# Optimization experiments

Hardware: AMD Instinct MI355X
Metric: run time of the kernel (lower is better)

The kernel has to match this reference:

```python
import jax, jax.numpy as jnp
import numpy as np
from jax import lax

EPS = 1e-05


def rmsnorm_axis1(x, w, eps=EPS):
    # RMS over channel axis (axis=1), scale by per-channel weight
    ms = jnp.mean(x * x, axis=1, keepdims=True)
    return x * lax.rsqrt(ms + eps) * w[None, :, None]


def dwconv1d(x, w, b, dilation):
    # x: [B, C, L]; w: [C, 1, K] depthwise (feature_group_count=C)
    pad = (w.shape[-1] - 1) // 2 * dilation
    y = lax.conv_general_dilated(
        x, w, window_strides=(1,), padding=[(pad, pad)],
        rhs_dilation=(dilation,), dimension_numbers=('NCH', 'OIH', 'NCH'),
        feature_group_count=x.shape[1])
    return y + b[None, :, None]


def setup_inputs() -> dict:
    key = jax.random.key(0)
    ks = jax.random.split(key, 12)
    B, C, L, K = 16, 512, 2048, 3
    s = 1.0 / np.sqrt(C)
    return {
        'number_log': jax.random.normal(ks[0], (B,), jnp.float32),
        'x': jax.random.normal(ks[1], (B, C, L), jnp.float32),
        'pre_w': jnp.ones((C,), jnp.float32),
        'conv_w': jax.random.normal(ks[2], (C, 1, K), jnp.float32) * 0.3,
        'conv_b': jnp.zeros((C,), jnp.float32),
        'conv1_w': jax.random.normal(ks[3], (C, 1, K), jnp.float32) * 0.3,
        'conv1_b': jnp.zeros((C,), jnp.float32),
        'conv2_w': jax.random.normal(ks[4], (C, 1, K), jnp.float32) * 0.3,
        'conv2_b': jnp.zeros((C,), jnp.float32),
        'gate_w': jax.random.normal(ks[5], (C, C), jnp.float32) * s,
        'gate_b': jnp.zeros((C,), jnp.float32),
        'post_w': jnp.ones((C,), jnp.float32),
        'logits_w': jax.random.normal(ks[6], (1, C, 1), jnp.float32) * s,
    }


def reference(number_log, x, pre_w, conv_w, conv_b, conv1_w, conv1_b,
              conv2_w, conv2_b, gate_w, gate_b, post_w, logits_w):
    # pre_norm over channel axis
    x_norm = rmsnorm_axis1(x, pre_w)
    # three dilated depthwise conv branches, summed
    x_d = (dwconv1d(x_norm, conv_w, conv_b, 1)
           + dwconv1d(x_norm, conv1_w, conv1_b, 2)
           + dwconv1d(x_norm, conv2_w, conv2_b, 4))
    # gate: Linear over channel dim of transposed input, SiLU
    gate = jax.nn.silu(jnp.einsum('bcl,dc->bdl', x_norm, gate_w)
                       + gate_b[None, :, None])
    x_d = rmsnorm_axis1(x_d * gate, post_w)
    # logits: 1x1 conv C->1, no bias
    out = jnp.einsum('bcl,oc->bol', x + x_d, logits_w[:, :, 0])
    return out
```

## Files before the change

kernel.cpp:

```cpp
#include <hip/hip_runtime.h>
#include <hip/hip_bf16.h>

#define BB 16
#define CC 512
#define LL 2048

typedef float f32x4 __attribute__((ext_vector_type(4)));
typedef short s16x8 __attribute__((ext_vector_type(8)));

static __device__ __forceinline__ float bf2f(unsigned short u) {
    union { unsigned int i; float f; } v; v.i = ((unsigned int)u) << 16; return v.f;
}
static __device__ __forceinline__ unsigned short f2bf(float f) {
    union { float fv; unsigned int i; } v; v.fv = f;
    unsigned int x = v.i;
    return (unsigned short)((x + 0x7FFFu + ((x >> 16) & 1u)) >> 16);
}

__global__ void k0_cast(const float* __restrict__ gw, unsigned short* __restrict__ gwb) {
    int i = blockIdx.x * 256 + threadIdx.x;
    if (i < CC * CC) gwb[i] = f2bf(gw[i]);
}

#define K1_ST 524
__global__ __launch_bounds__(256) void k1_rms_t(
    const float* __restrict__ x, const float* __restrict__ pre_w,
    unsigned short* __restrict__ xnt, float* __restrict__ invr) {
    __shared__ float tile[32 * K1_ST];
    __shared__ float red[32 * 33];
    __shared__ float pwS[CC];
    __shared__ float ivS[32];
    const int tid = threadIdx.x;
    const int b  = blockIdx.x >> 6;
    const int lt = blockIdx.x & 63;
    const int l0 = lt * 32;
    const float* xb = x + (size_t)(b * CC) * LL + l0;

    for (int i = tid; i < CC; i += 256) pwS[i] = pre_w[i];

    const int lq = tid & 7;
    const int cr = tid >> 3;
    f32x4 ssq = {0.f, 0.f, 0.f, 0.f};
    #pragma unroll
    for (int p = 0; p < 16; ++p) {
        int c = p * 32 + cr;
        f32x4 v = *(const f32x4*)(xb + (size_t)c * LL + lq * 4);
        #pragma unroll
        for (int r = 0; r < 4; ++r) {
            ssq[r] += v[r] * v[r];
            tile[(lq * 4 + r) * K1_ST + c] = v[r];
        }
    }
    #pragma unroll
    for (int r = 0; r < 4; ++r) red[(lq * 4 + r) * 33 + cr] = ssq[r];
    __syncthreads();
    if (tid < 32) {
        float s = 0.f;
        #pragma unroll
        for (int g = 0; g < 32; ++g) s += red[tid * 33 + g];
        float iv = rsqrtf(s * (1.0f / CC) + 1e-5f);
        ivS[tid] = iv;
        invr[b * LL + l0 + tid] = iv;
    }
    __syncthreads();
    unsigned short* xo = xnt + ((size_t)b * LL + l0) * CC;
    #pragma unroll
    for (int p = 0; p < 16; ++p) {
        int q = p * 256 + tid;
        int l = q >> 7, cq = (q & 127) * 4;
        f32x4 t = *(const f32x4*)&tile[l * K1_ST + cq];
        f32x4 w = *(const f32x4*)&pwS[cq];
        float iv = ivS[l];
        ushort4 o;
        o.x = f2bf(t[0] * iv * w[0]);
        o.y = f2bf(t[1] * iv * w[1]);
        o.z = f2bf(t[2] * iv * w[2]);
        o.w = f2bf(t[3] * iv * w[3]);
        *(ushort4*)(xo + (size_t)l * CC + cq) = o;
    }
}

__global__ __launch_bounds__(512) void k2_gemm(
    const unsigned short* __restrict__ gwb,
    const unsigned short* __restrict__ xnt,
    const float* __restrict__ gate_b,
    unsigned short* __restrict__ gate) {
    __shared__ unsigned short As[2][256 * 64];
    __shared__ unsigned short Bs[2][256 * 64];
    const int tid = threadIdx.x;
    const int w = tid >> 6, lane = tid & 63;
    const int lo = lane & 15, hi = lane >> 4;
    const int wm = w >> 2, wn = w & 3;
    const int nt = blockIdx.x, mt = blockIdx.y, b = blockIdx.z;
    const int m0 = mt * 256, n0 = nt * 256;
    const unsigned short* Ab = gwb;
    const unsigned short* Bb = xnt + (size_t)b * LL * CC;

    #define K2_STAGE(buf, kt)                                                        \
        {                                                                            \
            int k0_ = (kt) * 64;                                                     \
            _Pragma("unroll")                                                        \
            for (int s = 0; s < 4; ++s) {                                            \
                int g = tid + s * 512;                                               \
                int row = g >> 3, col8 = (g & 7) * 8;                                \
                __builtin_amdgcn_global_load_lds(                                    \
                    (const __attribute__((address_space(1))) void*)(Ab + (size_t)(m0 + row) * CC + k0_ + col8), \
                    (__attribute__((address_space(3))) void*)(&As[buf][g * 8]),      \
                    16, 0, 0);                                                       \
                __builtin_amdgcn_global_load_lds(                                    \
                    (const __attribute__((address_space(1))) void*)(Bb + (size_t)(n0 + row) * CC + k0_ + col8), \
                    (__attribute__((address_space(3))) void*)(&Bs[buf][g * 8]),      \
                    16, 0, 0);                                                       \
            }                                                                        \
        }

    f32x4 acc[8][4] = {};
    K2_STAGE(0, 0);
    __syncthreads();

    for (int kt = 0; kt < 8; ++kt) {
        const int cur = kt & 1;
        if (kt < 7) K2_STAGE(cur ^ 1, kt + 1);
        #pragma unroll
        for (int kk = 0; kk < 2; ++kk) {
            s16x8 af[8], bf[4];
            #pragma unroll
            for (int mi = 0; mi < 8; ++mi)
                af[mi] = *(const s16x8*)(&As[cur][(wm * 128 + mi * 16 + lo) * 64 + kk * 32 + hi * 8]);
            #pragma unroll
            for (int ni = 0; ni < 4; ++ni)
                bf[ni] = *(const s16x8*)(&Bs[cur][(wn * 64 + ni * 16 + lo) * 64 + kk * 32 + hi * 8]);
            #pragma unroll
            for (int mi = 0; mi < 8; ++mi)
                #pragma unroll
                for (int ni = 0; ni < 4; ++ni)
                    acc[mi][ni] = __builtin_amdgcn_mfma_f32_16x16x32_bf16(
                        af[mi], bf[ni], acc[mi][ni], 0, 0, 0);
        }
        __syncthreads();
    }

    #pragma unroll
    for (int mi = 0; mi < 8; ++mi) {
        #pragma unroll
        for (int ni = 0; ni < 4; ++ni) {
            int n = n0 + wn * 64 + ni * 16 + lo;
            int d0 = m0 + wm * 128 + mi * 16 + hi * 4;
            #pragma unroll
            for (int r = 0; r < 4; ++r) {
                int d = d0 + r;
                float z = acc[mi][ni][r] + gate_b[d];
                float s = z / (1.0f + __expf(-z));
                gate[((size_t)(b * CC + d)) * LL + n] = f2bf(s);
            }
        }
    }
}

__global__ __launch_bounds__(256) void k3a(
    const float* __restrict__ x, const float* __restrict__ invr,
    const unsigned short* __restrict__ gate,
    const float* __restrict__ cw0, const float* __restrict__ cb0,
    const float* __restrict__ cw1, const float* __restrict__ cb1,
    const float* __restrict__ cw2, const float* __restrict__ cb2,
    const float* __restrict__ pre_w, const float* __restrict__ post_w,
    const float* __restrict__ lw, float* __restrict__ part) {
    __shared__ float tapS[64][8];
    __shared__ float biasS[64], preS[64], lwS[64], pwlwS[64];
    __shared__ float ivs[136];
    __shared__ float red[8][128][3];
    const int tid = threadIdx.x;
    const int lt = blockIdx.x;
    const int cc = blockIdx.y;
    const int b  = blockIdx.z;
    const int l0 = lt * 128;
    const int c0 = cc * 64;

    if (tid < 64) {
        int c = c0 + tid;
        float w10 = cw0[c*3], w11 = cw0[c*3+1], w12 = cw0[c*3+2];
        float w20 = cw1[c*3], w21 = cw1[c*3+1], w22 = cw1[c*3+2];
        float w40 = cw2[c*3], w41 = cw2[c*3+1], w42 = cw2[c*3+2];
        tapS[tid][0] = w40; tapS[tid][1] = w20; tapS[tid][2] = w10;
        tapS[tid][3] = w11 + w21 + w41;
        tapS[tid][4] = w12; tapS[tid][5] = w22; tapS[tid][6] = w42;
        biasS[tid] = cb0[c] + cb1[c] + cb2[c];
        preS[tid]  = pre_w[c];
        float lwc = lw[c];
        lwS[tid] = lwc;
        pwlwS[tid] = post_w[c] * lwc;
    }
    if (tid < 136) {
        int lg = l0 - 4 + tid;
        ivs[tid] = (lg >= 0 && lg < LL) ? invr[b * LL + lg] : 0.f;
    }
    __syncthreads();

    const int li = tid & 31, ci = tid >> 5;
    const int lq = l0 + li * 4;
    float iv[12];
    #pragma unroll
    for (int j = 0; j < 12; ++j) iv[j] = ivs[li * 4 + j];

    const int ia = (lq - 4 < 0) ? 0 : lq - 4;
    const int ic = (lq + 4 > LL - 4) ? LL - 4 : lq + 4;

    float ass[4] = {}, adp[4] = {}, adx[4] = {};
    const float* xbase = x + ((size_t)(b * CC + c0)) * LL;
    const unsigned short* gbase = gate + ((size_t)(b * CC + c0)) * LL;

    #pragma unroll
    for (int j = 0; j < 8; ++j) {
        const int cl = ci * 8 + j;
        const float* xr = xbase + (size_t)cl * LL;
        f32x4 xa = *(const f32x4*)(xr + ia);
        f32x4 xm = *(const f32x4*)(xr + lq);
        f32x4 xc = *(const f32x4*)(xr + ic);
        uint2 gu = *(const uint2*)(gbase + (size_t)cl * LL + lq);
        float g[4];
        g[0] = bf2f((unsigned short)(gu.x & 0xffff));
        g[1] = bf2f((unsigned short)(gu.x >> 16));
        g[2] = bf2f((unsigned short)(gu.y & 0xffff));
        g[3] = bf2f((unsigned short)(gu.y >> 16));
        float z[12];
        #pragma unroll
        for (int r = 0; r < 4; ++r) {
            z[r]     = xa[r] * iv[r];
            z[r + 4] = xm[r] * iv[r + 4];
            z[r + 8] = xc[r] * iv[r + 8];
        }
        const float t0 = tapS[cl][0], t1 = tapS[cl][1], t2 = tapS[cl][2],
                    t3 = tapS[cl][3], t4 = tapS[cl][4], t5 = tapS[cl][5],
                    t6 = tapS[cl][6];
        const float pre = preS[cl], bias = biasS[cl], pwlw = pwlwS[cl], lwc = lwS[cl];
        #pragma unroll
        for (int k = 0; k < 4; ++k) {
            float s = t0 * z[k] + t1 * z[k + 2] + t2 * z[k + 3] + t3 * z[k + 4]
                    + t4 * z[k + 5] + t5 * z[k + 6] + t6 * z[k + 8];
            float p = (pre * s + bias) * g[k];
            ass[k] += p * p;
            adp[k] += p * pwlw;
            adx[k] += xm[k] * lwc;
        }
    }
    #pragma unroll
    for (int k = 0; k < 4; ++k) {
        red[ci][li * 4 + k][0] = ass[k];
        red[ci][li * 4 + k][1] = adp[k];
        red[ci][li * 4 + k][2] = adx[k];
    }
    __syncthreads();
    if (tid < 128) {
        float s0 = 0.f, s1 = 0.f, s2 = 0.f;
        #pragma unroll
        for (int g2 = 0; g2 < 8; ++g2) {
            s0 += red[g2][tid][0];
            s1 += red[g2][tid][1];
            s2 += red[g2][tid][2];
        }
        float* pp = part + (((size_t)(b * 8 + cc)) * LL + l0 + tid) * 3;
        pp[0] = s0; pp[1] = s1; pp[2] = s2;
    }
}

__global__ __launch_bounds__(256) void k3b(
    const float* __restrict__ part, float* __restrict__ out) {
    int gl = blockIdx.x * 256 + threadIdx.x;
    int b = gl >> 11, l = gl & 2047;
    float s0 = 0.f, s1 = 0.f, s2 = 0.f;
    #pragma unroll
    for (int cc2 = 0; cc2 < 8; ++cc2) {
        const float* pp = part + (((size_t)(b * 8 + cc2)) * LL + l) * 3;
        s0 += pp[0]; s1 += pp[1]; s2 += pp[2];
    }
    out[gl] = s2 + rsqrtf(s0 * (1.0f / CC) + 1e-5f) * s1;
}

extern "C" void kernel_launch(void* const* d_in, const int* in_sizes, int n_in,
                              void* d_out, int out_size, void* d_ws, size_t ws_size,
                              hipStream_t stream) {
    const float* x      = (const float*)d_in[1];
    const float* pre_w  = (const float*)d_in[2];
    const float* cw0    = (const float*)d_in[3];
    const float* cb0    = (const float*)d_in[4];
    const float* cw1    = (const float*)d_in[5];
    const float* cb1    = (const float*)d_in[6];
    const float* cw2    = (const float*)d_in[7];
    const float* cb2    = (const float*)d_in[8];
    const float* gw     = (const float*)d_in[9];
    const float* gb     = (const float*)d_in[10];
    const float* post_w = (const float*)d_in[11];
    const float* lw     = (const float*)d_in[12];
    float* out = (float*)d_out;

    char* ws = (char*)d_ws;
    unsigned short* gwb  = (unsigned short*)(ws);
    unsigned short* xnt  = (unsigned short*)(ws + 524288);
    float*          invr = (float*)(ws + 524288 + 33554432);
    unsigned short* gate = (unsigned short*)(ws + 524288 + 33554432 + 131072);
    float*          part = (float*)(ws + 524288);

    hipLaunchKernelGGL(k0_cast,  dim3((CC * CC + 255) / 256), dim3(256), 0, stream, gw, gwb);
    hipLaunchKernelGGL(k1_rms_t, dim3(BB * (LL / 32)),        dim3(256), 0, stream, x, pre_w, xnt, invr);
    hipLaunchKernelGGL(k2_gemm,  dim3(LL / 256, CC / 256, BB), dim3(512), 0, stream, gwb, xnt, gb, gate);
    hipLaunchKernelGGL(k3a,      dim3(LL / 128, CC / 64, BB), dim3(256), 0, stream,
                       x, invr, gate, cw0, cb0, cw1, cb1, cw2, cb2, pre_w, post_w, lw, part);
    hipLaunchKernelGGL(k3b,      dim3(BB * LL / 256),         dim3(256), 0, stream, part, out);
}
```

Before: 85.23 us.

## Stage k1 tile in bf16 and software-pipeline the gate GEMM with swizzled LDS

k1 now stores the transposed tile in LDS as bf16 instead of fp32, which halves shared memory and lets the output pass move 8-element vectors. This adds an extra rounding of x before normalisation. The gate GEMM splits each k-step into four phases that interleave LDS fragment reads, async global-to-LDS prefetch of the next tile, and MFMA bursts under raised wave priority, with explicit barriers and waitcnts. It also XOR-swizzles the LDS k offsets to cut bank conflicts and requests 2 blocks per CU in the launch bounds, which may raise register pressure.

```diff
diff --git a/kernel.cpp b/kernel.cpp
--- a/kernel.cpp
+++ b/kernel.cpp
@@ -22,11 +22,11 @@
     if (i < CC * CC) gwb[i] = f2bf(gw[i]);
 }
 
-#define K1_ST 524
+#define K1_ST 520
 __global__ __launch_bounds__(256) void k1_rms_t(
     const float* __restrict__ x, const float* __restrict__ pre_w,
     unsigned short* __restrict__ xnt, float* __restrict__ invr) {
-    __shared__ float tile[32 * K1_ST];
+    __shared__ unsigned short tile[32 * K1_ST];
     __shared__ float red[32 * 33];
     __shared__ float pwS[CC];
     __shared__ float ivS[32];
@@ -48,7 +48,7 @@
         #pragma unroll
         for (int r = 0; r < 4; ++r) {
             ssq[r] += v[r] * v[r];
-            tile[(lq * 4 + r) * K1_ST + c] = v[r];
+            tile[(lq * 4 + r) * K1_ST + c] = f2bf(v[r]);
         }
     }
     #pragma unroll
@@ -65,22 +65,24 @@
     __syncthreads();
     unsigned short* xo = xnt + ((size_t)b * LL + l0) * CC;
     #pragma unroll
-    for (int p = 0; p < 16; ++p) {
-        int q = p * 256 + tid;
-        int l = q >> 7, cq = (q & 127) * 4;
-        f32x4 t = *(const f32x4*)&tile[l * K1_ST + cq];
-        f32x4 w = *(const f32x4*)&pwS[cq];
+    for (int p = 0; p < 8; ++p) {
+        int g = p * 256 + tid;
+        int l = g >> 6, c8 = (g & 63) * 8;
+        s16x8 t = *(const s16x8*)&tile[l * K1_ST + c8];
+        f32x4 w0 = *(const f32x4*)&pwS[c8];
+        f32x4 w1 = *(const f32x4*)&pwS[c8 + 4];
         float iv = ivS[l];
-        ushort4 o;
-        o.x = f2bf(t[0] * iv * w[0]);
-        o.y = f2bf(t[1] * iv * w[1]);
-        o.z = f2bf(t[2] * iv * w[2]);
-        o.w = f2bf(t[3] * iv * w[3]);
-        *(ushort4*)(xo + (size_t)l * CC + cq) = o;
-    }
-}
-
-__global__ __launch_bounds__(512) void k2_gemm(
+        s16x8 o;
+        #pragma unroll
+        for (int r = 0; r < 4; ++r) {
+            o[r]     = (short)f2bf(bf2f((unsigned short)t[r])     * iv * w0[r]);
+            o[r + 4] = (short)f2bf(bf2f((unsigned short)t[r + 4]) * iv * w1[r]);
+        }
+        *(s16x8*)(xo + (size_t)l * CC + c8) = o;
+    }
+}
+
+__global__ __launch_bounds__(512, 2) void k2_gemm(
     const unsigned short* __restrict__ gwb,
     const unsigned short* __restrict__ xnt,
     const float* __restrict__ gate_b,
@@ -96,48 +98,70 @@
     const unsigned short* Ab = gwb;
     const unsigned short* Bb = xnt + (size_t)b * LL * CC;
 
-    #define K2_STAGE(buf, kt)                                                        \
+    #define K2_STG(pp, buf, kt_)                                                     \
         {                                                                            \
-            int k0_ = (kt) * 64;                                                     \
-            _Pragma("unroll")                                                        \
-            for (int s = 0; s < 4; ++s) {                                            \
-                int g = tid + s * 512;                                               \
-                int row = g >> 3, col8 = (g & 7) * 8;                                \
-                __builtin_amdgcn_global_load_lds(                                    \
-                    (const __attribute__((address_space(1))) void*)(Ab + (size_t)(m0 + row) * CC + k0_ + col8), \
-                    (__attribute__((address_space(3))) void*)(&As[buf][g * 8]),      \
-                    16, 0, 0);                                                       \
-                __builtin_amdgcn_global_load_lds(                                    \
-                    (const __attribute__((address_space(1))) void*)(Bb + (size_t)(n0 + row) * CC + k0_ + col8), \
-                    (__attribute__((address_space(3))) void*)(&Bs[buf][g * 8]),      \
-                    16, 0, 0);                                                       \
-            }                                                                        \
+            int g = (pp) * 512 + tid;                                                \
+            int row = g >> 3;                                                        \
+            int ks = ((g & 7) * 8) ^ ((row & 4) ? 16 : 0);                           \
+            __builtin_amdgcn_global_load_lds(                                        \
+                (const __attribute__((address_space(1))) void*)(Ab + (size_t)(m0 + row) * CC + (kt_) * 64 + ks), \
+                (__attribute__((address_space(3))) void*)(&As[buf][g * 8]),          \
+                16, 0, 0);                                                           \
+            __builtin_amdgcn_global_load_lds(                                        \
+                (const __attribute__((address_space(1))) void*)(Bb + (size_t)(n0 + row) * CC + (kt_) * 64 + ks), \
+                (__attribute__((address_space(3))) void*)(&Bs[buf][g * 8]),          \
+                16, 0, 0);                                                           \
         }
 
     f32x4 acc[8][4] = {};
-    K2_STAGE(0, 0);
-    __syncthreads();
-
+
+    #pragma unroll
+    for (int p = 0; p < 4; ++p) K2_STG(p, 0, 0);
+    asm volatile("s_waitcnt vmcnt(0)" ::: "memory");
+    __builtin_amdgcn_s_barrier();
+
+    #pragma unroll 2
     for (int kt = 0; kt < 8; ++kt) {
         const int cur = kt & 1;
-        if (kt < 7) K2_STAGE(cur ^ 1, kt + 1);
-        #pragma unroll
-        for (int kk = 0; kk < 2; ++kk) {
-            s16x8 af[8], bf[4];
+        s16x8 bf[4][2];
+        #pragma unroll
+        for (int p = 0; p < 4; ++p) {
+            s16x8 af[2][2];
             #pragma unroll
-            for (int mi = 0; mi < 8; ++mi)
-                af[mi] = *(const s16x8*)(&As[cur][(wm * 128 + mi * 16 + lo) * 64 + kk * 32 + hi * 8]);
+            for (int j = 0; j < 2; ++j) {
+                int row = wm * 128 + (p * 2 + j) * 16 + lo;
+                int kb = (row & 4) ? 16 : 0;
+                #pragma unroll
+                for (int kk = 0; kk < 2; ++kk)
+                    af[j][kk] = *(const s16x8*)(&As[cur][row * 64 + ((kk * 32 + hi * 8) ^ kb)]);
+            }
+            if (p == 0) {
+                #pragma unroll
+                for (int ni = 0; ni < 4; ++ni) {
+                    int row = wn * 64 + ni * 16 + lo;
+                    int kb = (row & 4) ? 16 : 0;
+                    #pragma unroll
+                    for (int kk = 0; kk < 2; ++kk)
+                        bf[ni][kk] = *(const s16x8*)(&Bs[cur][row * 64 + ((kk * 32 + hi * 8) ^ kb)]);
+                }
+            }
+            if (kt < 7) K2_STG(p, cur ^ 1, kt + 1);
+            __builtin_amdgcn_s_barrier();
+            asm volatile("s_waitcnt lgkmcnt(0)" ::: "memory");
+            __builtin_amdgcn_sched_barrier(0);
+            __builtin_amdgcn_s_setprio(1);
             #pragma unroll
-            for (int ni = 0; ni < 4; ++ni)
-                bf[ni] = *(const s16x8*)(&Bs[cur][(wn * 64 + ni * 16 + lo) * 64 + kk * 32 + hi * 8]);
-            #pragma unroll
-            for (int mi = 0; mi < 8; ++mi)
+            for (int j = 0; j < 2; ++j)
                 #pragma unroll
                 for (int ni = 0; ni < 4; ++ni)
-                    acc[mi][ni] = __builtin_amdgcn_mfma_f32_16x16x32_bf16(
-                        af[mi], bf[ni], acc[mi][ni], 0, 0, 0);
-        }
-        __syncthreads();
+                    #pragma unroll
+                    for (int kk = 0; kk < 2; ++kk)
+                        acc[p * 2 + j][ni] = __builtin_amdgcn_mfma_f32_16x16x32_bf16(
+                            af[j][kk], bf[ni][kk], acc[p * 2 + j][ni], 0, 0, 0);
+            __builtin_amdgcn_s_setprio(0);
+            if (p == 3) asm volatile("s_waitcnt vmcnt(0)" ::: "memory");
+            __builtin_amdgcn_s_barrier();
+        }
     }
 
     #pragma unroll
```

Result: faster. 79.16 us (-7.1%).
